# Optimization experiments

Hardware: AMD Instinct MI355X
Metric: run time of the kernel (lower is better)

Reference implementation:

```python
import jax, jax.numpy as jnp
import numpy as np

B, N, D, H = 2, 512, 32, 64

def custom_norm(x):
    # forward of tf custom_norm (stabilization only affects the gradient)
    return jnp.linalg.norm(x, axis=-1, keepdims=True)

def vecvec(a, b):
    """vector*vector -> (scalar, e12, e13, e23); identical math to the swizzle tensordot."""
    s = jnp.sum(a * b, axis=-1, keepdims=True)
    e12 = a[..., 0:1] * b[..., 1:2] - a[..., 1:2] * b[..., 0:1]
    e13 = a[..., 0:1] * b[..., 2:3] - a[..., 2:3] * b[..., 0:1]
    e23 = a[..., 1:2] * b[..., 2:3] - a[..., 2:3] * b[..., 1:2]
    return jnp.concatenate([s, e12, e13, e23], axis=-1)

def setup_inputs() -> dict:
    key = jax.random.key(0)
    ks = jax.random.split(key, 8)
    return {
        "positions": jax.random.normal(ks[0], (B, N, 3), jnp.float32),
        "values": jax.random.normal(ks[1], (B, N, D), jnp.float32),
        "W1": jax.random.normal(ks[2], (2, H), jnp.float32) * (2.0 / 2.0) ** 0.5,
        "b1": jnp.zeros((H,), jnp.float32),
        "W2": jax.random.normal(ks[3], (H, D), jnp.float32) * (2.0 / H) ** 0.5,
        "b2": jnp.zeros((D,), jnp.float32),
        "Ws1": jax.random.normal(ks[4], (D, H), jnp.float32) * (2.0 / D) ** 0.5,
        "bs1": jnp.zeros((H,), jnp.float32),
        "Ws2": jax.random.normal(ks[5], (H, 1), jnp.float32) * (2.0 / H) ** 0.5,
        "bs2": jnp.zeros((1,), jnp.float32),
    }

def reference(positions, values, W1, b1, W2, b2, Ws1, bs1, Ws2, bs2):
    # rank-2 tuple expansion (broadcast_indices): left varies last particle axis,
    # right varies second-to-last particle axis.
    r_left = positions[..., None, :, :]    # (B,1,N,3)
    r_right = positions[..., :, None, :]   # (B,N,1,3)
    prod = vecvec(r_left, r_right)         # (B,N,N,4) scalar + bivector
    # vecvec_invariants: scalar and bivector norm -> (B,N,N,2)
    invar = jnp.concatenate([prod[..., :1], custom_norm(prod[..., 1:4])], axis=-1)
    # merge_fun='mean' over the two tuple positions of the per-particle values
    neigh = 0.5 * (values[..., None, :, :] + values[..., :, None, :])  # (B,N,N,D)
    # value_net: Dense(H, relu) -> Dense(D)
    invar_values = jax.nn.relu(invar @ W1 + b1) @ W2 + b2              # (B,N,N,D)
    # join_fun='mean'
    joined = 0.5 * (invar_values + neigh)                              # (B,N,N,D)
    # score_net: Dense(H, relu) -> Dense(1)
    scores = jax.nn.relu(joined @ Ws1 + bs1) @ Ws2 + bs2               # (B,N,N,1)
    # reduce=True: softmax over all N*N*1 tuple scores per batch element
    attention = jax.nn.softmax(scores.reshape(scores.shape[0], -1), axis=-1)
    attention = attention.reshape(scores.shape)
    # weighted sum over both tuple axes (tuple_weights == 1, no weights input)
    return jnp.sum(attention * joined, axis=(-3, -2))                  # (B,D)
```

## Files before the change

### kernel.cpp

```cpp
#include <hip/hip_runtime.h>
#include <math.h>

#define BB 2
#define NN 512
#define DD 32
#define HH 64
#define JT 2
#define IPB 2
#define NBLK1 (BB*(NN/IPB)*JT)
#define NBLK3 (BB*NN)

#define SC_OFF  0
#define MF_OFF  (SC_OFF + BB*NN*NN)
#define WF_OFF  (MF_OFF + 2048)
#define W1F_OFF (WF_OFF + 1024)
#define PM2_OFF (W1F_OFF + 128)
#define PS2_OFF (PM2_OFF + NBLK1)
#define ST_OFF  (PS2_OFF + NBLK1)
#define AP_OFF  (ST_OFF + BB*2)
#define CS_OFF  (AP_OFF + BB*NN*HH)

typedef _Float16 half8 __attribute__((ext_vector_type(8)));
typedef float    f32x4 __attribute__((ext_vector_type(4)));

__device__ __forceinline__ half8 h8splat(float v) {
    _Float16 h = (_Float16)v;
    half8 r = {h,h,h,h,h,h,h,h};
    return r;
}

__device__ __forceinline__ void invar2(float pix, float piy, float piz,
                                       float pjx, float pjy, float pjz,
                                       float& s, float& cr) {
    s = pix*pjx + piy*pjy + piz*pjz;
    float e12 = pjx*piy - pjy*pix;
    float e13 = pjx*piz - pjz*pix;
    float e23 = pjy*piz - pjz*piy;
    cr = sqrtf(e12*e12 + e13*e13 + e23*e23);
}

#define R2 4096
#define R3 2048
#define R4 192
#define PREP_T (R2+R3+R4)

__global__ __launch_bounds__(256) void prep(const float* __restrict__ W1,
                                            const float* __restrict__ b1,
                                            const float* __restrict__ W2,
                                            const float* __restrict__ Ws1,
                                            float* __restrict__ ws) {
    int idx = blockIdx.x * 256 + threadIdx.x;
    if (idx < R2) {
        int e = idx;
        int t = e & 7, lane = (e >> 3) & 63, f = e >> 9;
        int cf = f >> 1, kh = f & 1;
        int k   = kh*32 + 8*(lane >> 4) + t;
        int col = cf*16 + (lane & 15);
        float acc = 0.f;
        #pragma unroll
        for (int d = 0; d < DD; d++) acc += W2[k*DD + d] * Ws1[d*HH + col];
        ((_Float16*)(ws + MF_OFF))[e] = (_Float16)(0.5f * acc);
    } else if (idx < R2+R3) {
        int e = idx - R2;
        int t = e & 7, lane = (e >> 3) & 63, cf = e >> 9;
        int k   = 8*(lane >> 4) + t;
        int col = cf*16 + (lane & 15);
        ((_Float16*)(ws + WF_OFF))[e] = (_Float16)(0.25f * Ws1[k*HH + col]);
    } else if (idx < R2+R3+R4) {
        int e = idx - R2 - R3;
        int t = e & 7, rest = e >> 3;
        int g = rest & 3, kh = (rest >> 2) & 1, arr = rest >> 3;
        int k = kh*32 + 8*g + t;
        float v = (arr == 0) ? W1[k] : (arr == 1) ? W1[HH + k] : b1[k];
        ((_Float16*)(ws + W1F_OFF))[e] = (_Float16)v;
    }
}

__global__ __launch_bounds__(256) void pass1(const float* __restrict__ pos,
                                             const float* __restrict__ values,
                                             const float* __restrict__ b2,
                                             const float* __restrict__ Ws1,
                                             const float* __restrict__ bs1,
                                             const float* __restrict__ Ws2,
                                             const float* __restrict__ bs2,
                                             float* __restrict__ ws) {
    __shared__ float uqc[IPB][HH];
    __shared__ float ws2l[HH];
    __shared__ float sm4[4], ss4[4];
    int blk = blockIdx.x;
    int jt = blk & 1;
    int ip = (blk >> 1) & 255;
    int b  = blk >> 9;
    int i0 = ip * IPB;
    int tid = threadIdx.x;
    int w    = tid >> 6;
    int lane = tid & 63;
    int g    = lane >> 4;
    int lr   = lane & 15;

    if (tid < IPB*HH) {
        int ii = tid >> 6, l = tid & 63;
        const float* vrow = values + (size_t)(b*NN + i0 + ii)*DD;
        float acc = bs1[l];
        #pragma unroll
        for (int d = 0; d < DD; d++) acc += (0.25f*vrow[d] + 0.5f*b2[d]) * Ws1[d*HH + l];
        uqc[ii][l] = acc;
        if (ii == 0) ws2l[l] = Ws2[l];
    }

    const half8* mf8 = (const half8*)(ws + MF_OFF);
    const half8* wf8 = (const half8*)(ws + WF_OFF);
    half8 Bf[4][2], Wf[4];
    #pragma unroll
    for (int cf = 0; cf < 4; cf++) {
        Bf[cf][0] = mf8[(cf*2 + 0)*64 + lane];
        Bf[cf][1] = mf8[(cf*2 + 1)*64 + lane];
        Wf[cf]    = wf8[cf*64 + lane];
    }
    const half8* w1f8 = (const half8*)(ws + W1F_OFF);
    half8 W1a[2], W1b[2], B1f[2];
    #pragma unroll
    for (int kh = 0; kh < 2; kh++) {
        W1a[kh] = w1f8[(0*2 + kh)*4 + g];
        W1b[kh] = w1f8[(1*2 + kh)*4 + g];
        B1f[kh] = w1f8[(2*2 + kh)*4 + g];
    }

    float pix[IPB], piy[IPB], piz[IPB];
    #pragma unroll
    for (int ii = 0; ii < IPB; ii++) {
        pix[ii] = pos[(b*NN+i0+ii)*3+0];
        piy[ii] = pos[(b*NN+i0+ii)*3+1];
        piz[ii] = pos[(b*NN+i0+ii)*3+2];
    }
    float bs2v = bs2[0];
    half8 z8 = h8splat(0.f);

    __syncthreads();

    float m_run = -INFINITY, s_run = 0.f;

    #pragma unroll
    for (int rf = 0; rf < 4; rf++) {
        int j_a = jt*256 + w*64 + rf*16 + lr;
        float pjx = pos[(b*NN+j_a)*3+0], pjy = pos[(b*NN+j_a)*3+1], pjz = pos[(b*NN+j_a)*3+2];
        const float* vj = values + (size_t)(b*NN + j_a)*DD + 8*g;
        half8 A2;
        #pragma unroll
        for (int t = 0; t < 8; t++) A2[t] = (_Float16)vj[t];

        #pragma unroll
        for (int ii = 0; ii < IPB; ii++) {
            float s, cr;
            invar2(pix[ii],piy[ii],piz[ii],pjx,pjy,pjz,s,cr);
            half8 s8 = h8splat(s), c8 = h8splat(cr);
            half8 A0 = __builtin_elementwise_max(W1a[0]*s8 + W1b[0]*c8 + B1f[0], z8);
            half8 A1 = __builtin_elementwise_max(W1a[1]*s8 + W1b[1]*c8 + B1f[1], z8);

            f32x4 c[4];
            #pragma unroll
            for (int cf = 0; cf < 4; cf++) {
                f32x4 z = {0.f, 0.f, 0.f, 0.f};
                z = __builtin_amdgcn_mfma_f32_16x16x32_f16(A0, Bf[cf][0], z, 0, 0, 0);
                z = __builtin_amdgcn_mfma_f32_16x16x32_f16(A1, Bf[cf][1], z, 0, 0, 0);
                c[cf] = __builtin_amdgcn_mfma_f32_16x16x32_f16(A2, Wf[cf], z, 0, 0, 0);
            }

            float part0 = 0.f, part1 = 0.f, part2 = 0.f, part3 = 0.f;
            #pragma unroll
            for (int cf = 0; cf < 4; cf++) {
                int lc = cf*16 + lr;
                float base = uqc[ii][lc];
                float w2v  = ws2l[lc];
                part0 += fmaxf(c[cf][0] + base, 0.f) * w2v;
                part1 += fmaxf(c[cf][1] + base, 0.f) * w2v;
                part2 += fmaxf(c[cf][2] + base, 0.f) * w2v;
                part3 += fmaxf(c[cf][3] + base, 0.f) * w2v;
            }
            #pragma unroll
            for (int m = 1; m < 16; m <<= 1) {
                part0 += __shfl_xor(part0, m);
                part1 += __shfl_xor(part1, m);
                part2 += __shfl_xor(part2, m);
                part3 += __shfl_xor(part3, m);
            }
            float x0 = part0 + bs2v, x1 = part1 + bs2v, x2 = part2 + bs2v, x3 = part3 + bs2v;
            if (lr == 0) {
                float4 outv; outv.x = x0; outv.y = x1; outv.z = x2; outv.w = x3;
                *(float4*)(ws + SC_OFF + (size_t)(b*NN + i0 + ii)*NN + jt*256 + w*64 + rf*16 + 4*g) = outv;
            }
            float mm = fmaxf(fmaxf(x0, x1), fmaxf(x2, x3));
            float nm = fmaxf(m_run, mm);
            s_run = s_run*__expf(m_run - nm)
                  + __expf(x0 - nm) + __expf(x1 - nm) + __expf(x2 - nm) + __expf(x3 - nm);
            m_run = nm;
        }
    }

    #pragma unroll
    for (int off = 16; off < 64; off <<= 1) {
        float om = __shfl_xor(m_run, off);
        float os = __shfl_xor(s_run, off);
        float nm = fmaxf(m_run, om);
        s_run = s_run*__expf(m_run - nm) + os*__expf(om - nm);
        m_run = nm;
    }
    if (lane == 0) { sm4[w] = m_run; ss4[w] = s_run; }
    __syncthreads();
    if (tid == 0) {
        float M0 = sm4[0], S0 = ss4[0];
        #pragma unroll
        for (int q = 1; q < 4; q++) {
            float nm = fmaxf(M0, sm4[q]);
            S0 = S0*__expf(M0 - nm) + ss4[q]*__expf(sm4[q] - nm);
            M0 = nm;
        }
        ws[PM2_OFF + blk] = M0;
        ws[PS2_OFF + blk] = S0;
    }
}

__global__ __launch_bounds__(256) void midk(float* __restrict__ ws) {
    __shared__ float red[8];
    int tid = threadIdx.x;
    int w = tid >> 6, lane = tid & 63;
    for (int b = 0; b < BB; b++) {
        float m = -INFINITY, s = 0.f;
        #pragma unroll
        for (int q = 0; q < 2; q++) {
            int p = b*512 + tid + q*256;
            float pm = ws[PM2_OFF + p], ps = ws[PS2_OFF + p];
            float nm = fmaxf(m, pm);
            s = s*__expf(m - nm) + ps*__expf(pm - nm);
            m = nm;
        }
        for (int off = 1; off < 64; off <<= 1) {
            float om = __shfl_xor(m, off);
            float os = __shfl_xor(s, off);
            float nm = fmaxf(m, om);
            s = s*__expf(m - nm) + os*__expf(om - nm);
            m = nm;
        }
        if (lane == 0) { red[w*2] = m; red[w*2+1] = s; }
        __syncthreads();
        if (tid == 0) {
            float M0 = red[0], S0 = red[1];
            #pragma unroll
            for (int q = 1; q < 4; q++) {
                float nm = fmaxf(M0, red[q*2]);
                S0 = S0*__expf(M0 - nm) + red[q*2+1]*__expf(red[q*2] - nm);
                M0 = nm;
            }
            ws[ST_OFF + b*2]     = M0;
            ws[ST_OFF + b*2 + 1] = 1.f / S0;
        }
        __syncthreads();
    }
}

__global__ __launch_bounds__(256) void pass3(const float* __restrict__ pos,
                                             const float* __restrict__ W1,
                                             const float* __restrict__ b1,
                                             float* __restrict__ ws) {
    __shared__ float sA[NN], cA[NN], wA[NN];
    __shared__ float Aw[4][HH];
    __shared__ float rs4[4];
    int blk = blockIdx.x;
    int b = blk >> 9;
    int i = blk & (NN-1);
    int tid = threadIdx.x;
    int w = tid >> 6, lane = tid & 63;

    float maxv = ws[ST_OFF + b*2], inv = ws[ST_OFF + b*2 + 1];
    float pix = pos[(b*NN+i)*3+0], piy = pos[(b*NN+i)*3+1], piz = pos[(b*NN+i)*3+2];
    const float* sc_row = ws + SC_OFF + (size_t)(b*NN + i)*NN;

    #pragma unroll
    for (int q = 0; q < 2; q++) {
        int j = tid + q*256;
        float pjx = pos[(b*NN+j)*3+0], pjy = pos[(b*NN+j)*3+1], pjz = pos[(b*NN+j)*3+2];
        float s, cr;
        invar2(pix,piy,piz,pjx,pjy,pjz,s,cr);
        float wgt = __expf(sc_row[j] - maxv) * inv;
        sA[j] = s; cA[j] = cr; wA[j] = wgt;
    }

    float w1a = W1[lane], w1b = W1[HH + lane], b1l = b1[lane];
    __syncthreads();
    float Ak = 0.f, rsum = 0.f;
    int p0 = w * 128;
    #pragma unroll 4
    for (int p = p0; p < p0 + 128; p++) {
        float s = sA[p], cr = cA[p], wgt = wA[p];
        float h = fmaxf(fmaf(w1a, s, fmaf(w1b, cr, b1l)), 0.f);
        Ak = fmaf(wgt, h, Ak);
        rsum += wgt;
    }
    Aw[w][lane] = Ak;
    if (lane == 0) rs4[w] = rsum;
    __syncthreads();
    if (tid < HH)
        ws[AP_OFF + ((size_t)(b*NN + i))*HH + tid] = Aw[0][tid] + Aw[1][tid] + Aw[2][tid] + Aw[3][tid];
    if (tid == 0)
        ws[CS_OFF + b*NN + i] = rs4[0] + rs4[1] + rs4[2] + rs4[3];
}

__global__ __launch_bounds__(256) void finalk(const float* __restrict__ values,
                                              const float* __restrict__ W2,
                                              const float* __restrict__ b2,
                                              const float* __restrict__ ws,
                                              float* __restrict__ out) {
    __shared__ float ap4[4][HH];
    __shared__ float vs8[8][DD];
    __shared__ float Ash[HH];
    int b = blockIdx.x;
    int tid = threadIdx.x;

    {
        int k = tid & 63, q = tid >> 6;
        const float* ap = ws + AP_OFF + (size_t)b*NN*HH;
        float a = 0.f;
        for (int i = q*128; i < q*128 + 128; i++) a += ap[(size_t)i*HH + k];
        ap4[q][k] = a;
    }
    {
        int d = tid & 31, q8 = tid >> 5;
        float v = 0.f;
        for (int n = q8*64; n < q8*64 + 64; n++)
            v += ws[CS_OFF + b*NN + n] * values[(size_t)(b*NN + n)*DD + d];
        vs8[q8][d] = v;
    }
    __syncthreads();
    if (tid < HH) Ash[tid] = ap4[0][tid] + ap4[1][tid] + ap4[2][tid] + ap4[3][tid];
    __syncthreads();
    if (tid < DD) {
        float vsum = 0.f;
        #pragma unroll
        for (int q = 0; q < 8; q++) vsum += vs8[q][tid];
        float aw = 0.f;
        #pragma unroll
        for (int k = 0; k < HH; k++) aw += Ash[k] * W2[k*DD + tid];
        out[b*DD + tid] = 0.5f*b2[tid] + 0.5f*aw + 0.5f*vsum;
    }
}

extern "C" void kernel_launch(void* const* d_in, const int* in_sizes, int n_in,
                              void* d_out, int out_size, void* d_ws, size_t ws_size,
                              hipStream_t stream) {
    (void)in_sizes; (void)n_in; (void)out_size; (void)ws_size;
    const float* pos    = (const float*)d_in[0];
    const float* values = (const float*)d_in[1];
    const float* W1     = (const float*)d_in[2];
    const float* b1     = (const float*)d_in[3];
    const float* W2     = (const float*)d_in[4];
    const float* b2     = (const float*)d_in[5];
    const float* Ws1    = (const float*)d_in[6];
    const float* bs1    = (const float*)d_in[7];
    const float* Ws2    = (const float*)d_in[8];
    const float* bs2    = (const float*)d_in[9];
    float* ws  = (float*)d_ws;
    float* out = (float*)d_out;

    prep  <<<(PREP_T + 255)/256, 256, 0, stream>>>(W1, b1, W2, Ws1, ws);
    pass1 <<<NBLK1, 256, 0, stream>>>(pos, values, b2, Ws1, bs1, Ws2, bs2, ws);
    midk  <<<1, 256, 0, stream>>>(ws);
    pass3 <<<NBLK3, 256, 0, stream>>>(pos, W1, b1, ws);
    finalk<<<BB, 256, 0, stream>>>(values, W2, b2, ws, out);
}
```

Baseline: 46.36 us.

## Fuse softmax-weighted hidden accumulation into pass1 and drop score buffer, midk, pass3

Pass1 now handles one row i per block instead of two. It keeps an online-softmax running accumulator of the first-layer hidden activations, weighted by exp(score - running max), and writes per-block partial vectors together with (max, sum) statistics. The finalk kernel merges these partials using the global max and normalizer. The full N×N score buffer, the midk kernel and the pass3 recomputation pass are all removed. This cuts two launches and a large global write/read, at the cost of more register pressure (16 accumulators plus shuffles) and halved reuse of the i-row per block.

```diff
diff --git a/kernel.cpp b/kernel.cpp
--- a/kernel.cpp
+++ b/kernel.cpp
@@ -6,19 +6,13 @@
 #define DD 32
 #define HH 64
 #define JT 2
-#define IPB 2
-#define NBLK1 (BB*(NN/IPB)*JT)
-#define NBLK3 (BB*NN)
-
-#define SC_OFF  0
-#define MF_OFF  (SC_OFF + BB*NN*NN)
+#define NBLK1 (BB*NN*JT)
+
+#define MF_OFF  0
 #define WF_OFF  (MF_OFF + 2048)
 #define W1F_OFF (WF_OFF + 1024)
-#define PM2_OFF (W1F_OFF + 128)
-#define PS2_OFF (PM2_OFF + NBLK1)
-#define ST_OFF  (PS2_OFF + NBLK1)
-#define AP_OFF  (ST_OFF + BB*2)
-#define CS_OFF  (AP_OFF + BB*NN*HH)
+#define ST2_OFF (W1F_OFF + 128)
+#define AR_OFF  (ST2_OFF + 4096)
 
 typedef _Float16 half8 __attribute__((ext_vector_type(8)));
 typedef float    f32x4 __attribute__((ext_vector_type(4)));
@@ -84,28 +78,27 @@
                                              const float* __restrict__ Ws2,
                                              const float* __restrict__ bs2,
                                              float* __restrict__ ws) {
-    __shared__ float uqc[IPB][HH];
+    __shared__ float uqc[HH];
     __shared__ float ws2l[HH];
-    __shared__ float sm4[4], ss4[4];
+    __shared__ float lA[4][HH];
+    __shared__ float lms[4][2];
     int blk = blockIdx.x;
     int jt = blk & 1;
-    int ip = (blk >> 1) & 255;
-    int b  = blk >> 9;
-    int i0 = ip * IPB;
+    int i  = (blk >> 1) & (NN-1);
+    int b  = blk >> 10;
     int tid = threadIdx.x;
     int w    = tid >> 6;
     int lane = tid & 63;
     int g    = lane >> 4;
     int lr   = lane & 15;
 
-    if (tid < IPB*HH) {
-        int ii = tid >> 6, l = tid & 63;
-        const float* vrow = values + (size_t)(b*NN + i0 + ii)*DD;
-        float acc = bs1[l];
-        #pragma unroll
-        for (int d = 0; d < DD; d++) acc += (0.25f*vrow[d] + 0.5f*b2[d]) * Ws1[d*HH + l];
-        uqc[ii][l] = acc;
-        if (ii == 0) ws2l[l] = Ws2[l];
+    if (tid < HH) {
+        const float* vrow = values + (size_t)(b*NN + i)*DD;
+        float acc = bs1[tid];
+        #pragma unroll
+        for (int d = 0; d < DD; d++) acc += (0.25f*vrow[d] + 0.5f*b2[d]) * Ws1[d*HH + tid];
+        uqc[tid]  = acc;
+        ws2l[tid] = Ws2[tid];
     }
 
     const half8* mf8 = (const half8*)(ws + MF_OFF);
@@ -126,19 +119,16 @@
         B1f[kh] = w1f8[(2*2 + kh)*4 + g];
     }
 
-    float pix[IPB], piy[IPB], piz[IPB];
-    #pragma unroll
-    for (int ii = 0; ii < IPB; ii++) {
-        pix[ii] = pos[(b*NN+i0+ii)*3+0];
-        piy[ii] = pos[(b*NN+i0+ii)*3+1];
-        piz[ii] = pos[(b*NN+i0+ii)*3+2];
-    }
+    float pix = pos[(b*NN+i)*3+0], piy = pos[(b*NN+i)*3+1], piz = pos[(b*NN+i)*3+2];
     float bs2v = bs2[0];
     half8 z8 = h8splat(0.f);
 
     __syncthreads();
 
     float m_run = -INFINITY, s_run = 0.f;
+    float Ak[16];
+    #pragma unroll
+    for (int t = 0; t < 16; t++) Ak[t] = 0.f;
 
     #pragma unroll
     for (int rf = 0; rf < 4; rf++) {
@@ -149,54 +139,64 @@
         #pragma unroll
         for (int t = 0; t < 8; t++) A2[t] = (_Float16)vj[t];
 
-        #pragma unroll
-        for (int ii = 0; ii < IPB; ii++) {
-            float s, cr;
-            invar2(pix[ii],piy[ii],piz[ii],pjx,pjy,pjz,s,cr);
-            half8 s8 = h8splat(s), c8 = h8splat(cr);
-            half8 A0 = __builtin_elementwise_max(W1a[0]*s8 + W1b[0]*c8 + B1f[0], z8);
-            half8 A1 = __builtin_elementwise_max(W1a[1]*s8 + W1b[1]*c8 + B1f[1], z8);
-
-            f32x4 c[4];
-            #pragma unroll
-            for (int cf = 0; cf < 4; cf++) {
-                f32x4 z = {0.f, 0.f, 0.f, 0.f};
-                z = __builtin_amdgcn_mfma_f32_16x16x32_f16(A0, Bf[cf][0], z, 0, 0, 0);
-                z = __builtin_amdgcn_mfma_f32_16x16x32_f16(A1, Bf[cf][1], z, 0, 0, 0);
-                c[cf] = __builtin_amdgcn_mfma_f32_16x16x32_f16(A2, Wf[cf], z, 0, 0, 0);
-            }
-
-            float part0 = 0.f, part1 = 0.f, part2 = 0.f, part3 = 0.f;
-            #pragma unroll
-            for (int cf = 0; cf < 4; cf++) {
-                int lc = cf*16 + lr;
-                float base = uqc[ii][lc];
-                float w2v  = ws2l[lc];
-                part0 += fmaxf(c[cf][0] + base, 0.f) * w2v;
-                part1 += fmaxf(c[cf][1] + base, 0.f) * w2v;
-                part2 += fmaxf(c[cf][2] + base, 0.f) * w2v;
-                part3 += fmaxf(c[cf][3] + base, 0.f) * w2v;
-            }
-            #pragma unroll
-            for (int m = 1; m < 16; m <<= 1) {
-                part0 += __shfl_xor(part0, m);
-                part1 += __shfl_xor(part1, m);
-                part2 += __shfl_xor(part2, m);
-                part3 += __shfl_xor(part3, m);
-            }
-            float x0 = part0 + bs2v, x1 = part1 + bs2v, x2 = part2 + bs2v, x3 = part3 + bs2v;
-            if (lr == 0) {
-                float4 outv; outv.x = x0; outv.y = x1; outv.z = x2; outv.w = x3;
-                *(float4*)(ws + SC_OFF + (size_t)(b*NN + i0 + ii)*NN + jt*256 + w*64 + rf*16 + 4*g) = outv;
-            }
-            float mm = fmaxf(fmaxf(x0, x1), fmaxf(x2, x3));
-            float nm = fmaxf(m_run, mm);
-            s_run = s_run*__expf(m_run - nm)
-                  + __expf(x0 - nm) + __expf(x1 - nm) + __expf(x2 - nm) + __expf(x3 - nm);
-            m_run = nm;
-        }
-    }
-
+        float s, cr;
+        invar2(pix,piy,piz,pjx,pjy,pjz,s,cr);
+        half8 s8 = h8splat(s), c8 = h8splat(cr);
+        half8 A0 = __builtin_elementwise_max(W1a[0]*s8 + W1b[0]*c8 + B1f[0], z8);
+        half8 A1 = __builtin_elementwise_max(W1a[1]*s8 + W1b[1]*c8 + B1f[1], z8);
+
+        f32x4 c[4];
+        #pragma unroll
+        for (int cf = 0; cf < 4; cf++) {
+            f32x4 z = {0.f, 0.f, 0.f, 0.f};
+            z = __builtin_amdgcn_mfma_f32_16x16x32_f16(A0, Bf[cf][0], z, 0, 0, 0);
+            z = __builtin_amdgcn_mfma_f32_16x16x32_f16(A1, Bf[cf][1], z, 0, 0, 0);
+            c[cf] = __builtin_amdgcn_mfma_f32_16x16x32_f16(A2, Wf[cf], z, 0, 0, 0);
+        }
+
+        float part0 = 0.f, part1 = 0.f, part2 = 0.f, part3 = 0.f;
+        #pragma unroll
+        for (int cf = 0; cf < 4; cf++) {
+            int lc = cf*16 + lr;
+            float base = uqc[lc];
+            float w2v  = ws2l[lc];
+            part0 += fmaxf(c[cf][0] + base, 0.f) * w2v;
+            part1 += fmaxf(c[cf][1] + base, 0.f) * w2v;
+            part2 += fmaxf(c[cf][2] + base, 0.f) * w2v;
+            part3 += fmaxf(c[cf][3] + base, 0.f) * w2v;
+        }
+        #pragma unroll
+        for (int m = 1; m < 16; m <<= 1) {
+            part0 += __shfl_xor(part0, m);
+            part1 += __shfl_xor(part1, m);
+            part2 += __shfl_xor(part2, m);
+            part3 += __shfl_xor(part3, m);
+        }
+        float x0 = part0 + bs2v, x1 = part1 + bs2v, x2 = part2 + bs2v, x3 = part3 + bs2v;
+
+        int src = (lr >> 2) << 4;
+        float y0 = __shfl(x0, src);
+        float y1 = __shfl(x1, src);
+        float y2 = __shfl(x2, src);
+        float y3 = __shfl(x3, src);
+        float t01 = (lr & 1) ? y1 : y0;
+        float t23 = (lr & 1) ? y3 : y2;
+        float x_own = (lr & 2) ? t23 : t01;
+
+        float mm = fmaxf(fmaxf(x0, x1), fmaxf(x2, x3));
+        float nm = fmaxf(m_run, mm);
+        float rsc = __expf(m_run - nm);
+        s_run = s_run*rsc
+              + __expf(x0 - nm) + __expf(x1 - nm) + __expf(x2 - nm) + __expf(x3 - nm);
+        float w_own = __expf(x_own - nm);
+        #pragma unroll
+        for (int t = 0; t < 8; t++) Ak[t]   = fmaf(Ak[t],   rsc, w_own * (float)A0[t]);
+        #pragma unroll
+        for (int t = 0; t < 8; t++) Ak[8+t] = fmaf(Ak[8+t], rsc, w_own * (float)A1[t]);
+        m_run = nm;
+    }
+
+    float mg = m_run;
     #pragma unroll
     for (int off = 16; off < 64; off <<= 1) {
         float om = __shfl_xor(m_run, off);
@@ -205,31 +205,59 @@
         s_run = s_run*__expf(m_run - nm) + os*__expf(om - nm);
         m_run = nm;
     }
-    if (lane == 0) { sm4[w] = m_run; ss4[w] = s_run; }
-    __syncthreads();
-    if (tid == 0) {
-        float M0 = sm4[0], S0 = ss4[0];
-        #pragma unroll
-        for (int q = 1; q < 4; q++) {
-            float nm = fmaxf(M0, sm4[q]);
-            S0 = S0*__expf(M0 - nm) + ss4[q]*__expf(sm4[q] - nm);
-            M0 = nm;
-        }
-        ws[PM2_OFF + blk] = M0;
-        ws[PS2_OFF + blk] = S0;
-    }
-}
-
-__global__ __launch_bounds__(256) void midk(float* __restrict__ ws) {
+    #pragma unroll
+    for (int t = 0; t < 16; t++) {
+        #pragma unroll
+        for (int msk = 1; msk < 16; msk <<= 1) Ak[t] += __shfl_xor(Ak[t], msk);
+    }
+    float gsc = __expf(mg - m_run);
+    if (lr == 0) {
+        #pragma unroll
+        for (int t = 0; t < 8; t++) lA[w][8*g + t]      = Ak[t]   * gsc;
+        #pragma unroll
+        for (int t = 0; t < 8; t++) lA[w][32 + 8*g + t] = Ak[8+t] * gsc;
+    }
+    if (lane == 0) { lms[w][0] = m_run; lms[w][1] = s_run; }
+    __syncthreads();
+
+    if (tid < HH) {
+        float m0 = lms[0][0], m1 = lms[1][0], m2 = lms[2][0], m3 = lms[3][0];
+        float mB = fmaxf(fmaxf(m0, m1), fmaxf(m2, m3));
+        float e0 = __expf(m0 - mB), e1 = __expf(m1 - mB);
+        float e2 = __expf(m2 - mB), e3 = __expf(m3 - mB);
+        float ar = lA[0][tid]*e0 + lA[1][tid]*e1 + lA[2][tid]*e2 + lA[3][tid]*e3;
+        ws[AR_OFF + (size_t)blk*HH + tid] = ar;
+        if (tid == 0) {
+            float sB = lms[0][1]*e0 + lms[1][1]*e1 + lms[2][1]*e2 + lms[3][1]*e3;
+            ws[ST2_OFF + blk*2]     = mB;
+            ws[ST2_OFF + blk*2 + 1] = sB;
+        }
+    }
+}
+
+__global__ __launch_bounds__(256) void finalk(const float* __restrict__ values,
+                                              const float* __restrict__ W2,
+                                              const float* __restrict__ b2,
+                                              const float* __restrict__ ws,
+                                              float* __restrict__ out) {
     __shared__ float red[8];
+    __shared__ float MS[2];
+    __shared__ float wf[NN*JT];
+    __shared__ float csh[NN];
+    __shared__ float vs8[8][DD];
+    __shared__ float as4[4][HH];
+    __shared__ float Ash[HH];
+    int b = blockIdx.x;
     int tid = threadIdx.x;
     int w = tid >> 6, lane = tid & 63;
-    for (int b = 0; b < BB; b++) {
+    const float* st2 = ws + ST2_OFF + (size_t)b*NN*JT*2;
+
+    {
         float m = -INFINITY, s = 0.f;
         #pragma unroll
-        for (int q = 0; q < 2; q++) {
-            int p = b*512 + tid + q*256;
-            float pm = ws[PM2_OFF + p], ps = ws[PS2_OFF + p];
+        for (int q = 0; q < 4; q++) {
+            int p = tid + q*256;
+            float pm = st2[p*2], ps = st2[p*2+1];
             float nm = fmaxf(m, pm);
             s = s*__expf(m - nm) + ps*__expf(pm - nm);
             m = nm;
@@ -242,96 +270,51 @@
             m = nm;
         }
         if (lane == 0) { red[w*2] = m; red[w*2+1] = s; }
-        __syncthreads();
-        if (tid == 0) {
-            float M0 = red[0], S0 = red[1];
-            #pragma unroll
-            for (int q = 1; q < 4; q++) {
-                float nm = fmaxf(M0, red[q*2]);
-                S0 = S0*__expf(M0 - nm) + red[q*2+1]*__expf(red[q*2] - nm);
-                M0 = nm;
-            }
-            ws[ST_OFF + b*2]     = M0;
-            ws[ST_OFF + b*2 + 1] = 1.f / S0;
-        }
-        __syncthreads();
-    }
-}
-
-__global__ __launch_bounds__(256) void pass3(const float* __restrict__ pos,
-                                             const float* __restrict__ W1,
-                                             const float* __restrict__ b1,
-                                             float* __restrict__ ws) {
-    __shared__ float sA[NN], cA[NN], wA[NN];
-    __shared__ float Aw[4][HH];
-    __shared__ float rs4[4];
-    int blk = blockIdx.x;
-    int b = blk >> 9;
-    int i = blk & (NN-1);
-    int tid = threadIdx.x;
-    int w = tid >> 6, lane = tid & 63;
-
-    float maxv = ws[ST_OFF + b*2], inv = ws[ST_OFF + b*2 + 1];
-    float pix = pos[(b*NN+i)*3+0], piy = pos[(b*NN+i)*3+1], piz = pos[(b*NN+i)*3+2];
-    const float* sc_row = ws + SC_OFF + (size_t)(b*NN + i)*NN;
-
+    }
+    __syncthreads();
+    if (tid == 0) {
+        float M0 = red[0], S0 = red[1];
+        #pragma unroll
+        for (int q = 1; q < 4; q++) {
+            float nm = fmaxf(M0, red[q*2]);
+            S0 = S0*__expf(M0 - nm) + red[q*2+1]*__expf(red[q*2] - nm);
+            M0 = nm;
+        }
+        MS[0] = M0; MS[1] = 1.f / S0;
+    }
+    __syncthreads();
+    float M = MS[0], invS = MS[1];
+
+    #pragma unroll
+    for (int q = 0; q < 4; q++) {
+        int p = tid + q*256;
+        wf[p] = __expf(st2[p*2] - M) * invS;
+    }
+    __syncthreads();
     #pragma unroll
     for (int q = 0; q < 2; q++) {
-        int j = tid + q*256;
-        float pjx = pos[(b*NN+j)*3+0], pjy = pos[(b*NN+j)*3+1], pjz = pos[(b*NN+j)*3+2];
-        float s, cr;
-        invar2(pix,piy,piz,pjx,pjy,pjz,s,cr);
-        float wgt = __expf(sc_row[j] - maxv) * inv;
-        sA[j] = s; cA[j] = cr; wA[j] = wgt;
-    }
-
-    float w1a = W1[lane], w1b = W1[HH + lane], b1l = b1[lane];
-    __syncthreads();
-    float Ak = 0.f, rsum = 0.f;
-    int p0 = w * 128;
-    #pragma unroll 4
-    for (int p = p0; p < p0 + 128; p++) {
-        float s = sA[p], cr = cA[p], wgt = wA[p];
-        float h = fmaxf(fmaf(w1a, s, fmaf(w1b, cr, b1l)), 0.f);
-        Ak = fmaf(wgt, h, Ak);
-        rsum += wgt;
-    }
-    Aw[w][lane] = Ak;
-    if (lane == 0) rs4[w] = rsum;
-    __syncthreads();
-    if (tid < HH)
-        ws[AP_OFF + ((size_t)(b*NN + i))*HH + tid] = Aw[0][tid] + Aw[1][tid] + Aw[2][tid] + Aw[3][tid];
-    if (tid == 0)
-        ws[CS_OFF + b*NN + i] = rs4[0] + rs4[1] + rs4[2] + rs4[3];
-}
-
-__global__ __launch_bounds__(256) void finalk(const float* __restrict__ values,
-                                              const float* __restrict__ W2,
-                                              const float* __restrict__ b2,
-                                              const float* __restrict__ ws,
-                                              float* __restrict__ out) {
-    __shared__ float ap4[4][HH];
-    __shared__ float vs8[8][DD];
-    __shared__ float Ash[HH];
-    int b = blockIdx.x;
-    int tid = threadIdx.x;
+        int i = tid + q*256;
+        csh[i] = st2[(2*i)*2+1]*wf[2*i] + st2[(2*i+1)*2+1]*wf[2*i+1];
+    }
+    __syncthreads();
 
     {
-        int k = tid & 63, q = tid >> 6;
-        const float* ap = ws + AP_OFF + (size_t)b*NN*HH;
+        int d = tid & 31, sl = tid >> 5;
+        float v = 0.f;
+        for (int i = sl*64; i < sl*64 + 64; i++)
+            v += csh[i] * values[(size_t)(b*NN + i)*DD + d];
+        vs8[sl][d] = v;
+    }
+    {
+        int k = tid & 63, sl = tid >> 6;
+        const float* ar = ws + AR_OFF + (size_t)b*NN*JT*HH;
         float a = 0.f;
-        for (int i = q*128; i < q*128 + 128; i++) a += ap[(size_t)i*HH + k];
-        ap4[q][k] = a;
-    }
-    {
-        int d = tid & 31, q8 = tid >> 5;
-        float v = 0.f;
-        for (int n = q8*64; n < q8*64 + 64; n++)
-            v += ws[CS_OFF + b*NN + n] * values[(size_t)(b*NN + n)*DD + d];
-        vs8[q8][d] = v;
-    }
-    __syncthreads();
-    if (tid < HH) Ash[tid] = ap4[0][tid] + ap4[1][tid] + ap4[2][tid] + ap4[3][tid];
+        for (int p = sl*256; p < sl*256 + 256; p++)
+            a += ar[(size_t)p*HH + k] * wf[p];
+        as4[sl][k] = a;
+    }
+    __syncthreads();
+    if (tid < HH) Ash[tid] = as4[0][tid] + as4[1][tid] + as4[2][tid] + as4[3][tid];
     __syncthreads();
     if (tid < DD) {
         float vsum = 0.f;
@@ -363,7 +346,5 @@
 
     prep  <<<(PREP_T + 255)/256, 256, 0, stream>>>(W1, b1, W2, Ws1, ws);
     pass1 <<<NBLK1, 256, 0, stream>>>(pos, values, b2, Ws1, bs1, Ws2, bs2, ws);
-    midk  <<<1, 256, 0, stream>>>(ws);
-    pass3 <<<NBLK3, 256, 0, stream>>>(pos, W1, b1, ws);
     finalk<<<BB, 256, 0, stream>>>(values, W2, b2, ws, out);
 }
```

Measured after the change: 45.54 us. Within noise of the previous version (-1.8%).
